# Kernel tuning notes

Hardware: AMD Instinct MI355X
Metric: run time of the kernel (lower is better)

The kernel has to match this reference:

```python
import jax, jax.numpy as jnp
import numpy as np

NUM_HEADS = 16
HEAD_SIZE = 64
HIDDEN = NUM_HEADS * HEAD_SIZE  # 1024


def setup_inputs() -> dict:
    key = jax.random.key(0)
    ks = jax.random.split(key, 9)
    B, S1, S2 = 8, 1024, 1024
    scale = 1.0 / np.sqrt(HIDDEN)
    inp = {
        "s1_hidden_states": jax.random.normal(ks[0], (B, S1, HIDDEN), jnp.float32),
        "s2_hidden_states": jax.random.normal(ks[1], (B, S2, HIDDEN), jnp.float32),
        "s2_attention_mask": jnp.zeros((B, 1, 1, S2), jnp.float32),
        "Wq": jax.random.normal(ks[2], (HIDDEN, HIDDEN), jnp.float32) * scale,
        "bq": jnp.zeros((HIDDEN,), jnp.float32),
        "Wk": jax.random.normal(ks[3], (HIDDEN, HIDDEN), jnp.float32) * scale,
        "bk": jnp.zeros((HIDDEN,), jnp.float32),
        "Wv": jax.random.normal(ks[4], (HIDDEN, HIDDEN), jnp.float32) * scale,
        "bv": jnp.zeros((HIDDEN,), jnp.float32),
        "cl_att": 1,
    }
    return inp


def _split_heads(x):
    # [B, S, H*D] -> [B, H, S, D]
    B, S, _ = x.shape
    return x.reshape(B, S, NUM_HEADS, HEAD_SIZE).transpose(0, 2, 1, 3)


def reference(s1_hidden_states, s2_hidden_states, s2_attention_mask,
              Wq, bq, Wk, bk, Wv, bv, cl_att):
    q = _split_heads(s1_hidden_states @ Wq + bq)  # [B,H,S1,D]
    k = _split_heads(s2_hidden_states @ Wk + bk)  # [B,H,S2,D]
    v = _split_heads(s2_hidden_states @ Wv + bv)  # [B,H,S2,D]

    scores = jnp.einsum("bhqd,bhkd->bhqk", q, k) / np.sqrt(HEAD_SIZE)
    scores = scores + s2_attention_mask  # broadcast [B,1,1,S2]
    probs = jax.nn.softmax(scores, axis=-1)
    if cl_att:
        probs = jax.nn.softmax(1.0 - probs + s2_attention_mask, axis=-1)
    # dropout is identity in eval/reference mode
    ctx = jnp.einsum("bhqk,bhkd->bhqd", probs, v)  # [B,H,S1,D]
    B, _, S1, _ = ctx.shape
    return ctx.transpose(0, 2, 1, 3).reshape(B, S1, HIDDEN)
```

## Files before the change

### kernel.cpp

```cpp
#include <hip/hip_runtime.h>
#include <hip/hip_bf16.h>

typedef unsigned short u16;
typedef __attribute__((ext_vector_type(8))) short bf16x8;
typedef __attribute__((ext_vector_type(4))) float f32x4;
typedef __attribute__((ext_vector_type(4))) unsigned u32x4;

#define L2E 1.4426950408889634f

__device__ __forceinline__ u16 f2bf(float f) {
  unsigned u = __float_as_uint(f);
  u = u + 0x7fffu + ((u >> 16) & 1u);
  return (u16)(u >> 16);
}
__device__ __forceinline__ unsigned cvtpk(float a, float b) {
  unsigned r;
  asm("v_cvt_pk_bf16_f32 %0, %1, %2" : "=v"(r) : "v"(a), "v"(b));
  return r;
}
__device__ __forceinline__ float lo16(unsigned v) { return __uint_as_float(v << 16); }
__device__ __forceinline__ float hi16(unsigned v) { return __uint_as_float(v & 0xffff0000u); }

__global__ void conv2_f32_bf16(const float* __restrict__ a, const float* __restrict__ b,
                               u16* __restrict__ o, int n4a, int n4tot) {
  int i = blockIdx.x * blockDim.x + threadIdx.x;
  int stride = gridDim.x * blockDim.x;
  for (; i < n4tot; i += stride) {
    float4 v = (i < n4a) ? ((const float4*)a)[i] : ((const float4*)b)[i - n4a];
    ushort4 ov = make_ushort4(f2bf(v.x), f2bf(v.y), f2bf(v.z), f2bf(v.w));
    ((ushort4*)o)[i] = ov;
  }
}

__global__ void wtrans3(const float* __restrict__ Wq, const float* __restrict__ Wk,
                        const float* __restrict__ Wv,
                        u16* __restrict__ Wtq, u16* __restrict__ Wtk, u16* __restrict__ Wtv) {
  int z = blockIdx.z;
  const float* W = (z == 0) ? Wq : (z == 1) ? Wk : Wv;
  u16* Wt = (z == 0) ? Wtq : (z == 1) ? Wtk : Wtv;
  __shared__ float T[32][33];
  int k0 = blockIdx.y * 32, n0 = blockIdx.x * 32;
  int tx = threadIdx.x, ty = threadIdx.y;
  #pragma unroll
  for (int j = 0; j < 4; ++j) T[ty + 8*j][tx] = W[(size_t)(k0 + ty + 8*j) * 1024 + n0 + tx];
  __syncthreads();
  #pragma unroll
  for (int j = 0; j < 4; ++j) Wt[(size_t)(n0 + ty + 8*j) * 1024 + k0 + tx] = f2bf(T[tx][ty + 8*j]);
}

__global__ __launch_bounds__(256) void qkv_gemm3(const u16* __restrict__ X1, const u16* __restrict__ X2,
                                                 const u16* __restrict__ Wtq, const u16* __restrict__ Wtk,
                                                 const u16* __restrict__ Wtv,
                                                 const float* __restrict__ bq, const float* __restrict__ bk,
                                                 const float* __restrict__ bv,
                                                 u16* __restrict__ Qo, u16* __restrict__ Ko, u16* __restrict__ Vo) {
  int bid = blockIdx.x;
  int xcd = bid & 7, idx = bid >> 3;
  int nblk = idx & 7, pair = idx >> 3;
  int zy = xcd * 24 + pair;
  int z = zy >> 6, y = zy & 63;
  int m0 = y * 128, n0 = nblk * 128;

  const u16* X   = (z == 0) ? X1 : X2;
  const u16* Wt  = (z == 0) ? Wtq : (z == 1) ? Wtk : Wtv;
  const float* bias = (z == 0) ? bq : (z == 1) ? bk : bv;
  u16* outp = (z == 0) ? Qo : (z == 1) ? Ko : Vo;

  __shared__ __align__(16) u16 As[2][128 * 32];
  __shared__ __align__(16) u16 Bs[2][128 * 32];
  int tid = threadIdx.x;
  int w = tid >> 6, l = tid & 63;
  int wm = w >> 1, wn = w & 1;
  int lq = l & 15, g = l >> 4;
  const int4* Xs = (const int4*)X;
  const int4* Ws = (const int4*)Wt;

#define QSTAGE(bi, kt) do { _Pragma("unroll")                                                \
    for (int c_ = 0; c_ < 2; ++c_) {                                                        \
      int i_ = c_ * 256 + tid;                                      \
      int row_ = i_ >> 2, kc_ = (i_ & 3) ^ ((row_ >> 1) & 3);                               \
      __builtin_amdgcn_global_load_lds(                                                     \
          (const __attribute__((address_space(1))) void*)&Xs[(size_t)(m0 + row_) * 128 + (kt) * 4 + kc_], \
          (__attribute__((address_space(3))) void*)&((int4*)As[bi])[i_], 16, 0, 0);         \
      __builtin_amdgcn_global_load_lds(                                                     \
          (const __attribute__((address_space(1))) void*)&Ws[(size_t)(n0 + row_) * 128 + (kt) * 4 + kc_], \
          (__attribute__((address_space(3))) void*)&((int4*)Bs[bi])[i_], 16, 0, 0);         \
    } } while (0)

  int aOff[4], bOff[4];
  #pragma unroll
  for (int mc = 0; mc < 4; ++mc) {
    int rowA = wm * 64 + mc * 16 + lq;
    aOff[mc] = rowA * 32 + ((g ^ ((rowA >> 1) & 3)) * 8);
    int rowB = wn * 64 + mc * 16 + lq;
    bOff[mc] = rowB * 32 + ((g ^ ((rowB >> 1) & 3)) * 8);
  }

  f32x4 acc[4][4] = {};
  QSTAGE(0, 0);
  __syncthreads();
  int cur = 0;
  for (int kt = 0; kt < 32; ++kt) {
    if (kt < 31) QSTAGE(cur ^ 1, kt + 1);
    bf16x8 a[4], bb[4];
    #pragma unroll
    for (int mc = 0; mc < 4; ++mc) a[mc]  = *(const bf16x8*)&As[cur][aOff[mc]];
    #pragma unroll
    for (int nc = 0; nc < 4; ++nc) bb[nc] = *(const bf16x8*)&Bs[cur][bOff[nc]];
    #pragma unroll
    for (int mc = 0; mc < 4; ++mc)
      #pragma unroll
      for (int nc = 0; nc < 4; ++nc)
        acc[mc][nc] = __builtin_amdgcn_mfma_f32_16x16x32_bf16(a[mc], bb[nc], acc[mc][nc], 0, 0, 0);
    __syncthreads();
    cur ^= 1;
  }
#undef QSTAGE
  #pragma unroll
  for (int nc = 0; nc < 4; ++nc) {
    int n = n0 + wn * 64 + nc * 16 + lq;
    float bvv = bias[n];
    int h = n >> 6, d = n & 63;
    #pragma unroll
    for (int mc = 0; mc < 4; ++mc) {
      int srow_base = m0 + wm * 64 + mc * 16 + g * 4;
      if (z == 2) {
        int b = srow_base >> 10, s = srow_base & 1023;
        ushort4 vv;
        vv.x = f2bf(acc[mc][nc][0] + bvv);
        vv.y = f2bf(acc[mc][nc][1] + bvv);
        vv.z = f2bf(acc[mc][nc][2] + bvv);
        vv.w = f2bf(acc[mc][nc][3] + bvv);
        *(ushort4*)&outp[((size_t)((b * 16 + h) * 64 + d)) * 1024 + s] = vv;
      } else {
        #pragma unroll
        for (int r = 0; r < 4; ++r) {
          int sm = srow_base + r;
          int b = sm >> 10, s = sm & 1023;
          outp[((size_t)((b * 16 + h) * 1024 + s)) * 64 + d] = f2bf(acc[mc][nc][r] + bvv);
        }
      }
    }
  }
}

__global__ __launch_bounds__(256, 2) void attn13(const u16* __restrict__ Q, const u16* __restrict__ K,
                                                 const u16* __restrict__ Vt, const float* __restrict__ mask,
                                                 const int* __restrict__ clp, float* __restrict__ out) {
  __shared__ __align__(16) u16 KVl[2][8192];
  __shared__ __align__(16) float maskL2[1024];
  __shared__ float z1p[4][32];
  __shared__ float z2p[4][32];

  int bid = blockIdx.x;
  int xcd = bid & 7, idx = bid >> 3;
  int bh = xcd * 16 + (idx >> 5);
  int qt = idx & 31;
  int b = bh >> 4, h = bh & 15;
  int tid = threadIdx.x;
  int w = tid >> 6, l = tid & 63;
  int lq = l & 15, g = l >> 4;
  int qb = qt * 32;

  const u16* Kb = K + (size_t)bh * 65536;
  const u16* Vb = Vt + (size_t)bh * 65536;
  int cl = clp[0];

  const u16* kS[4]; int kD[4];
  #pragma unroll
  for (int c_ = 0; c_ < 4; ++c_) {
    int i_ = c_ * 256 + tid, row_ = i_ >> 3, ch_ = i_ & 7;
    int f_ = (row_ & 3) | ((((row_ >> 3) ^ (row_ >> 4)) & 1) << 2);
    kS[c_] = Kb + row_ * 64 + (ch_ ^ f_) * 8;
    kD[c_] = i_ * 8;
  }
  const u16* vS[4]; int vD[4];
  #pragma unroll
  for (int c_ = 0; c_ < 4; ++c_) {
    int i_ = c_ * 256 + tid, row_ = i_ >> 4, ch_ = i_ & 15;
    vS[c_] = Vb + row_ * 1024 + (ch_ ^ (row_ & 15)) * 8;
    vD[c_] = i_ * 8;
  }

#define STAGE_K(bi, t) do { _Pragma("unroll")                                                 \
    for (int c_ = 0; c_ < 4; ++c_)                                                           \
      __builtin_amdgcn_global_load_lds(                                                      \
        (const __attribute__((address_space(1))) void*)(kS[c_] + (t) * 8192),                \
        (__attribute__((address_space(3))) void*)&KVl[bi][kD[c_]], 16, 0, 0); } while (0)

#define STAGE_V(bi, t) do { _Pragma("unroll")                                                 \
    for (int c_ = 0; c_ < 4; ++c_)                                                           \
      __builtin_amdgcn_global_load_lds(                                                      \
        (const __attribute__((address_space(1))) void*)(vS[c_] + (t) * 128),                 \
        (__attribute__((address_space(3))) void*)&KVl[bi][vD[c_]], 16, 0, 0); } while (0)

  STAGE_K(0, 0);

  for (int i = tid; i < 1024; i += 256) maskL2[i] = mask[b * 1024 + i] * L2E;

  bf16x8 qf[2][2];
  #pragma unroll
  for (int qg = 0; qg < 2; ++qg) {
    const u16* Qp = Q + ((size_t)bh * 1024 + qb + qg * 16 + lq) * 64 + g * 8;
    qf[qg][0] = *(const bf16x8*)Qp;
    qf[qg][1] = *(const bf16x8*)(Qp + 32);
  }

  int kOff[2][2];
  #pragma unroll
  for (int c = 0; c < 2; ++c) {
    int row128 = w * 32 + ((lq >> 2) << 3) + c * 4 + (lq & 3);
    int F = (row128 & 3) | ((((row128 >> 3) ^ (row128 >> 4)) & 1) << 2);
    kOff[c][0] = row128 * 64 + ((g ^ F) * 8);
    kOff[c][1] = row128 * 64 + (((g + 4) ^ F) * 8);
  }
  int vOff[4];
  #pragma unroll
  for (int dc = 0; dc < 4; ++dc) {
    int row = dc * 16 + lq;
    vOff[dc] = row * 128 + (((w * 4 + g) ^ (row & 15)) * 8);
  }
  int mBase = w * 32 + g * 8;

  __syncthreads();

  const float sl2e = 0.125f * L2E;
  unsigned sp[64];
  float z1[2] = {0.f, 0.f};
  int cur = 0;
  #pragma unroll
  for (int t = 0; t < 8; ++t) {
    if (t < 7) STAGE_K(cur ^ 1, t + 1);
    else       STAGE_V(0, 0);
    #pragma unroll
    for (int c = 0; c < 2; ++c) {
      bf16x8 kf0 = *(const bf16x8*)&KVl[cur][kOff[c][0]];
      bf16x8 kf1 = *(const bf16x8*)&KVl[cur][kOff[c][1]];
      const float4 mk = *(const float4*)&maskL2[t * 128 + mBase + c * 4];
      #pragma unroll
      for (int qg = 0; qg < 2; ++qg) {
        f32x4 tt = {0.f, 0.f, 0.f, 0.f};
        tt = __builtin_amdgcn_mfma_f32_16x16x32_bf16(kf0, qf[qg][0], tt, 0, 0, 0);
        tt = __builtin_amdgcn_mfma_f32_16x16x32_bf16(kf1, qf[qg][1], tt, 0, 0, 0);
        float e0 = __builtin_amdgcn_exp2f(fmaf(tt[0], sl2e, mk.x));
        float e1 = __builtin_amdgcn_exp2f(fmaf(tt[1], sl2e, mk.y));
        float e2 = __builtin_amdgcn_exp2f(fmaf(tt[2], sl2e, mk.z));
        float e3 = __builtin_amdgcn_exp2f(fmaf(tt[3], sl2e, mk.w));
        z1[qg] += (e0 + e1) + (e2 + e3);
        sp[t * 8 + qg * 4 + c * 2 + 0] = cvtpk(e0, e1);
        sp[t * 8 + qg * 4 + c * 2 + 1] = cvtpk(e2, e3);
      }
    }
    __syncthreads();
    cur ^= 1;
  }

  #pragma unroll
  for (int qg = 0; qg < 2; ++qg) {
    z1[qg] += __shfl_xor(z1[qg], 16);
    z1[qg] += __shfl_xor(z1[qg], 32);
  }
  if (l < 16) { z1p[w][l] = z1[0]; z1p[w][16 + l] = z1[1]; }
  __syncthreads();
  float cr[2];
  #pragma unroll
  for (int qg = 0; qg < 2; ++qg) {
    int q = qg * 16 + lq;
    float Z1 = (z1p[0][q] + z1p[1][q]) + (z1p[2][q] + z1p[3][q]);
    cr[qg] = L2E * __builtin_amdgcn_rcpf(Z1);
  }

  f32x4 acc[2][4] = {};
  float z2[2] = {0.f, 0.f};
  #pragma unroll
  for (int t = 0; t < 8; ++t) {
    if (t < 7) STAGE_V((t + 1) & 1, t + 1);
    u32x4 pk[2];
    #pragma unroll
    for (int qg = 0; qg < 2; ++qg) {
      if (cl) {
        #pragma unroll
        for (int j = 0; j < 4; ++j) {
          unsigned e = sp[t * 8 + qg * 4 + j];
          float mkA = maskL2[t * 128 + mBase + 2 * j];
          float mkB = maskL2[t * 128 + mBase + 2 * j + 1];
          float pA = __builtin_amdgcn_exp2f(fmaf(-cr[qg], lo16(e), mkA));
          float pB = __builtin_amdgcn_exp2f(fmaf(-cr[qg], hi16(e), mkB));
          z2[qg] += pA + pB;
          pk[qg][j] = cvtpk(pA, pB);
        }
      } else {
        pk[qg] = *(u32x4*)&sp[t * 8 + qg * 4];
      }
    }
    #pragma unroll
    for (int dc = 0; dc < 4; ++dc) {
      bf16x8 vf = *(const bf16x8*)&KVl[t & 1][vOff[dc]];
      #pragma unroll
      for (int qg = 0; qg < 2; ++qg)
        acc[qg][dc] = __builtin_amdgcn_mfma_f32_16x16x32_bf16(
            __builtin_bit_cast(bf16x8, pk[qg]), vf, acc[qg][dc], 0, 0, 0);
    }
    if (t < 7) __syncthreads();
  }

  #pragma unroll
  for (int qg = 0; qg < 2; ++qg) {
    z2[qg] += __shfl_xor(z2[qg], 16);
    z2[qg] += __shfl_xor(z2[qg], 32);
  }
  if (l < 16) { z2p[w][l] = z2[0]; z2p[w][16 + l] = z2[1]; }
  float* redF = (float*)&KVl[0][0];
  if (w > 0) {
    #pragma unroll
    for (int qg = 0; qg < 2; ++qg)
      #pragma unroll
      for (int dc = 0; dc < 4; ++dc)
        #pragma unroll
        for (int r = 0; r < 4; ++r)
          redF[(w - 1) * 2176 + (qg * 16 + g * 4 + r) * 68 + dc * 16 + lq] = acc[qg][dc][r];
  }
  __syncthreads();
  if (w == 0) {
    #pragma unroll
    for (int qg = 0; qg < 2; ++qg) {
      #pragma unroll
      for (int r = 0; r < 4; ++r) {
        int q = qg * 16 + g * 4 + r;
        float phi;
        if (cl) {
          float Z2 = (z2p[0][q] + z2p[1][q]) + (z2p[2][q] + z2p[3][q]);
          phi = __builtin_amdgcn_rcpf(Z2);
        } else {
          float Z1 = (z1p[0][q] + z1p[1][q]) + (z1p[2][q] + z1p[3][q]);
          phi = __builtin_amdgcn_rcpf(Z1);
        }
        size_t orow = ((size_t)(b * 1024 + qb + q)) * 1024 + h * 64;
        #pragma unroll
        for (int dc = 0; dc < 4; ++dc) {
          int dq = q * 68 + dc * 16 + lq;
          float o = acc[qg][dc][r] + redF[dq] + redF[2176 + dq] + redF[4352 + dq];
          out[orow + dc * 16 + lq] = o * phi;
        }
      }
    }
  }
#undef STAGE_K
#undef STAGE_V
}

extern "C" void kernel_launch(void* const* d_in, const int* in_sizes, int n_in,
                              void* d_out, int out_size, void* d_ws, size_t ws_size,
                              hipStream_t stream) {
  const float* s1   = (const float*)d_in[0];
  const float* s2   = (const float*)d_in[1];
  const float* mask = (const float*)d_in[2];
  const float* Wq   = (const float*)d_in[3];
  const float* bq   = (const float*)d_in[4];
  const float* Wk   = (const float*)d_in[5];
  const float* bk   = (const float*)d_in[6];
  const float* Wv   = (const float*)d_in[7];
  const float* bv   = (const float*)d_in[8];
  const int*   cl   = (const int*)d_in[9];
  float* out = (float*)d_out;

  u16* ws  = (u16*)d_ws;
  const size_t M1 = 1024 * 1024;
  u16* X1  = ws;
  u16* Wtq = ws + 16 * M1;
  u16* Wtk = Wtq + M1;
  u16* Wtv = Wtk + M1;
  u16* Qb  = Wtv + M1;
  u16* Kb  = Qb + 8 * M1;
  u16* Vtb = Kb + 8 * M1;
  u16* X2  = ws + 8 * M1;

  conv2_f32_bf16<<<2048, 256, 0, stream>>>(s1, s2, X1, 2097152, 4194304);
  wtrans3<<<dim3(32, 32, 3), dim3(32, 8), 0, stream>>>(Wq, Wk, Wv, Wtq, Wtk, Wtv);
  qkv_gemm3<<<1536, 256, 0, stream>>>(X1, X2, Wtq, Wtk, Wtv, bq, bk, bv, Qb, Kb, Vtb);
  attn13<<<4096, 256, 0, stream>>>(Qb, Kb, Vtb, mask, cl, out);
}
```

Measured before the change: 177.2 us.

## Fuse K and V projections in one GEMM block to share X2 tiles

```diff
diff --git a/kernel.cpp b/kernel.cpp
--- a/kernel.cpp
+++ b/kernel.cpp
@@ -48,43 +48,45 @@
   for (int j = 0; j < 4; ++j) Wt[(size_t)(n0 + ty + 8*j) * 1024 + k0 + tx] = f2bf(T[tx][ty + 8*j]);
 }
 
-__global__ __launch_bounds__(256) void qkv_gemm3(const u16* __restrict__ X1, const u16* __restrict__ X2,
+__global__ __launch_bounds__(256) void qkv_fused(const u16* __restrict__ X1, const u16* __restrict__ X2,
                                                  const u16* __restrict__ Wtq, const u16* __restrict__ Wtk,
                                                  const u16* __restrict__ Wtv,
                                                  const float* __restrict__ bq, const float* __restrict__ bk,
                                                  const float* __restrict__ bv,
                                                  u16* __restrict__ Qo, u16* __restrict__ Ko, u16* __restrict__ Vo) {
+  __shared__ __align__(16) u16 As[2][4096];
+  __shared__ __align__(16) u16 Bs[2][4096];
+  __shared__ __align__(16) u16 Cs[2][4096];
+
   int bid = blockIdx.x;
   int xcd = bid & 7, idx = bid >> 3;
-  int nblk = idx & 7, pair = idx >> 3;
-  int zy = xcd * 24 + pair;
-  int z = zy >> 6, y = zy & 63;
+  int kind = idx >> 6, sub = idx & 63;
+  int y = xcd * 8 + (sub >> 3), nblk = sub & 7;
   int m0 = y * 128, n0 = nblk * 128;
 
-  const u16* X   = (z == 0) ? X1 : X2;
-  const u16* Wt  = (z == 0) ? Wtq : (z == 1) ? Wtk : Wtv;
-  const float* bias = (z == 0) ? bq : (z == 1) ? bk : bv;
-  u16* outp = (z == 0) ? Qo : (z == 1) ? Ko : Vo;
-
-  __shared__ __align__(16) u16 As[2][128 * 32];
-  __shared__ __align__(16) u16 Bs[2][128 * 32];
   int tid = threadIdx.x;
   int w = tid >> 6, l = tid & 63;
   int wm = w >> 1, wn = w & 1;
   int lq = l & 15, g = l >> 4;
-  const int4* Xs = (const int4*)X;
-  const int4* Ws = (const int4*)Wt;
-
-#define QSTAGE(bi, kt) do { _Pragma("unroll")                                                \
+
+  const int4* Xs = (const int4*)(kind ? X2 : X1);
+  const int4* W0 = (const int4*)(kind ? Wtk : Wtq);
+  const int4* W1 = (const int4*)Wtv;
+
+#define FSTAGE(bi, kt) do { _Pragma("unroll")                                               \
     for (int c_ = 0; c_ < 2; ++c_) {                                                        \
-      int i_ = c_ * 256 + tid;                                      \
+      int i_ = c_ * 256 + tid;                                                              \
       int row_ = i_ >> 2, kc_ = (i_ & 3) ^ ((row_ >> 1) & 3);                               \
       __builtin_amdgcn_global_load_lds(                                                     \
           (const __attribute__((address_space(1))) void*)&Xs[(size_t)(m0 + row_) * 128 + (kt) * 4 + kc_], \
           (__attribute__((address_space(3))) void*)&((int4*)As[bi])[i_], 16, 0, 0);         \
       __builtin_amdgcn_global_load_lds(                                                     \
-          (const __attribute__((address_space(1))) void*)&Ws[(size_t)(n0 + row_) * 128 + (kt) * 4 + kc_], \
+          (const __attribute__((address_space(1))) void*)&W0[(size_t)(n0 + row_) * 128 + (kt) * 4 + kc_], \
           (__attribute__((address_space(3))) void*)&((int4*)Bs[bi])[i_], 16, 0, 0);         \
+      if (kind)                                                                             \
+        __builtin_amdgcn_global_load_lds(                                                   \
+            (const __attribute__((address_space(1))) void*)&W1[(size_t)(n0 + row_) * 128 + (kt) * 4 + kc_], \
+            (__attribute__((address_space(3))) void*)&((int4*)Cs[bi])[i_], 16, 0, 0);       \
     } } while (0)
 
   int aOff[4], bOff[4];
@@ -96,55 +98,76 @@
     bOff[mc] = rowB * 32 + ((g ^ ((rowB >> 1) & 3)) * 8);
   }
 
-  f32x4 acc[4][4] = {};
-  QSTAGE(0, 0);
+  f32x4 acc0[4][4] = {};
+  f32x4 acc1[4][4] = {};
+  FSTAGE(0, 0);
   __syncthreads();
   int cur = 0;
   for (int kt = 0; kt < 32; ++kt) {
-    if (kt < 31) QSTAGE(cur ^ 1, kt + 1);
-    bf16x8 a[4], bb[4];
+    if (kt < 31) FSTAGE(cur ^ 1, kt + 1);
+    bf16x8 a[4], b0[4];
     #pragma unroll
     for (int mc = 0; mc < 4; ++mc) a[mc]  = *(const bf16x8*)&As[cur][aOff[mc]];
     #pragma unroll
-    for (int nc = 0; nc < 4; ++nc) bb[nc] = *(const bf16x8*)&Bs[cur][bOff[nc]];
+    for (int nc = 0; nc < 4; ++nc) b0[nc] = *(const bf16x8*)&Bs[cur][bOff[nc]];
     #pragma unroll
     for (int mc = 0; mc < 4; ++mc)
       #pragma unroll
       for (int nc = 0; nc < 4; ++nc)
-        acc[mc][nc] = __builtin_amdgcn_mfma_f32_16x16x32_bf16(a[mc], bb[nc], acc[mc][nc], 0, 0, 0);
+        acc0[mc][nc] = __builtin_amdgcn_mfma_f32_16x16x32_bf16(a[mc], b0[nc], acc0[mc][nc], 0, 0, 0);
+    if (kind) {
+      bf16x8 b1[4];
+      #pragma unroll
+      for (int nc = 0; nc < 4; ++nc) b1[nc] = *(const bf16x8*)&Cs[cur][bOff[nc]];
+      #pragma unroll
+      for (int mc = 0; mc < 4; ++mc)
+        #pragma unroll
+        for (int nc = 0; nc < 4; ++nc)
+          acc1[mc][nc] = __builtin_amdgcn_mfma_f32_16x16x32_bf16(a[mc], b1[nc], acc1[mc][nc], 0, 0, 0);
+    }
     __syncthreads();
     cur ^= 1;
   }
-#undef QSTAGE
+#undef FSTAGE
   #pragma unroll
   for (int nc = 0; nc < 4; ++nc) {
     int n = n0 + wn * 64 + nc * 16 + lq;
-    float bvv = bias[n];
     int h = n >> 6, d = n & 63;
-    #pragma unroll
-    for (int mc = 0; mc < 4; ++mc) {
-      int srow_base = m0 + wm * 64 + mc * 16 + g * 4;
-      if (z == 2) {
-        int b = srow_base >> 10, s = srow_base & 1023;
-        ushort4 vv;
-        vv.x = f2bf(acc[mc][nc][0] + bvv);
-        vv.y = f2bf(acc[mc][nc][1] + bvv);
-        vv.z = f2bf(acc[mc][nc][2] + bvv);
-        vv.w = f2bf(acc[mc][nc][3] + bvv);
-        *(ushort4*)&outp[((size_t)((b * 16 + h) * 64 + d)) * 1024 + s] = vv;
-      } else {
+    if (kind == 0) {
+      float bvv = bq[n];
+      #pragma unroll
+      for (int mc = 0; mc < 4; ++mc) {
+        int srow_base = m0 + wm * 64 + mc * 16 + g * 4;
         #pragma unroll
         for (int r = 0; r < 4; ++r) {
           int sm = srow_base + r;
           int b = sm >> 10, s = sm & 1023;
-          outp[((size_t)((b * 16 + h) * 1024 + s)) * 64 + d] = f2bf(acc[mc][nc][r] + bvv);
+          Qo[((size_t)((b * 16 + h) * 1024 + s)) * 64 + d] = f2bf(acc0[mc][nc][r] + bvv);
         }
       }
-    }
-  }
-}
-
-__global__ __launch_bounds__(256, 2) void attn13(const u16* __restrict__ Q, const u16* __restrict__ K,
+    } else {
+      float bkk = bk[n], bvv = bv[n];
+      #pragma unroll
+      for (int mc = 0; mc < 4; ++mc) {
+        int srow_base = m0 + wm * 64 + mc * 16 + g * 4;
+        int b = srow_base >> 10, s = srow_base & 1023;
+        #pragma unroll
+        for (int r = 0; r < 4; ++r) {
+          int sm = srow_base + r;
+          Ko[((size_t)((b * 16 + h) * 1024 + (sm & 1023))) * 64 + d] = f2bf(acc0[mc][nc][r] + bkk);
+        }
+        ushort4 vv;
+        vv.x = f2bf(acc1[mc][nc][0] + bvv);
+        vv.y = f2bf(acc1[mc][nc][1] + bvv);
+        vv.z = f2bf(acc1[mc][nc][2] + bvv);
+        vv.w = f2bf(acc1[mc][nc][3] + bvv);
+        *(ushort4*)&Vo[((size_t)((b * 16 + h) * 64 + d)) * 1024 + s] = vv;
+      }
+    }
+  }
+}
+
+__global__ __launch_bounds__(256, 2) void attn16(const u16* __restrict__ Q, const u16* __restrict__ K,
                                                  const u16* __restrict__ Vt, const float* __restrict__ mask,
                                                  const int* __restrict__ clp, float* __restrict__ out) {
   __shared__ __align__(16) u16 KVl[2][8192];
@@ -310,6 +333,7 @@
     z2[qg] += __shfl_xor(z2[qg], 32);
   }
   if (l < 16) { z2p[w][l] = z2[0]; z2p[w][16 + l] = z2[1]; }
+  __syncthreads();
   float* redF = (float*)&KVl[0][0];
   if (w > 0) {
     #pragma unroll
@@ -377,6 +401,6 @@
 
   conv2_f32_bf16<<<2048, 256, 0, stream>>>(s1, s2, X1, 2097152, 4194304);
   wtrans3<<<dim3(32, 32, 3), dim3(32, 8), 0, stream>>>(Wq, Wk, Wv, Wtq, Wtk, Wtv);
-  qkv_gemm3<<<1536, 256, 0, stream>>>(X1, X2, Wtq, Wtk, Wtv, bq, bk, bv, Qb, Kb, Vtb);
-  attn13<<<4096, 256, 0, stream>>>(Qb, Kb, Vtb, mask, cl, out);
-}
+  qkv_fused<<<1024, 256, 0, stream>>>(X1, X2, Wtq, Wtk, Wtv, bq, bk, bv, Qb, Kb, Vtb);
+  attn16<<<4096, 256, 0, stream>>>(Qb, Kb, Vtb, mask, cl, out);
+}
```

Result: slower. 209.8 us (+18.4%).
